# Kernel tuning notes

Measured on AMD Instinct MI355X. Metric: run time of the kernel, lower is better.

The kernel has to match this reference:

```python
import jax, jax.numpy as jnp
import numpy as np

B, H, W, D = 16, 48, 48, 384
EPS = 1e-5


def setup_inputs() -> dict:
    key = jax.random.key(0)
    ks = jax.random.split(key, 7)
    s_in = 1.0 / np.sqrt(D)
    s_pos = 1.0 / np.sqrt(2.0)
    return {
        "x": jax.random.normal(ks[0], (B, H, W, D), dtype=jnp.float32),
        "Wp": jax.random.uniform(ks[1], (2, D), minval=-s_pos, maxval=s_pos, dtype=jnp.float32),
        "bp": jax.random.uniform(ks[2], (D,), minval=-s_pos, maxval=s_pos, dtype=jnp.float32),
        "W1": jax.random.uniform(ks[3], (D, D), minval=-s_in, maxval=s_in, dtype=jnp.float32),
        "b1": jax.random.uniform(ks[4], (D,), minval=-s_in, maxval=s_in, dtype=jnp.float32),
        "W2": jax.random.uniform(ks[5], (D, D), minval=-s_in, maxval=s_in, dtype=jnp.float32),
        "b2": jax.random.uniform(ks[6], (D,), minval=-s_in, maxval=s_in, dtype=jnp.float32),
    }


def reference(x, Wp, bp, W1, b1, W2, b2):
    b, h, w, d = x.shape
    # positional encoding: (h, w, 2) -> Linear(2, d)
    ph = jnp.arange(h, dtype=jnp.float32)[:, None] * jnp.ones((1, w), jnp.float32)
    pw = jnp.arange(w, dtype=jnp.float32)[None, :] * jnp.ones((h, 1), jnp.float32)
    pos = jnp.stack((ph, pw), axis=-1)  # (h, w, 2)
    pos_enc = pos @ Wp + bp  # (h, w, d)
    x = x + pos_enc[None]
    xf = x.reshape(b, h * w, d)
    # unscaled self-attention: softmax(x x^T) x
    scores = jnp.einsum("bnd,bmd->bnm", xf, xf)  # (b, hw, hw)
    attn = jax.nn.softmax(scores, axis=-1)
    out = jnp.einsum("bnm,bmd->bnd", attn, xf)  # (b, hw, d)
    # MLP: Linear -> ReLU -> Linear
    out = jax.nn.relu(out @ W1 + b1) @ W2 + b2
    out = out.reshape(b, h, w, d) + x
    # layer_norm over [h, w, d] (no affine params)
    mean = jnp.mean(out, axis=(1, 2, 3), keepdims=True)
    var = jnp.var(out, axis=(1, 2, 3), keepdims=True)
    return (out - mean) * jax.lax.rsqrt(var + EPS)
```

## Files before the change

kernel.cpp:

```cpp
#include <hip/hip_runtime.h>
#include <cstdio>
#include <cstdint>

#define BB 16
#define HH 48
#define WW 48
#define DD 384
#define NTOK 2304
#define EPS 1e-5f
#define SZB 28311552u

typedef __attribute__((ext_vector_type(4))) float f32x4;
typedef __attribute__((ext_vector_type(8))) short bf16x8;
typedef __attribute__((ext_vector_type(4))) short bf16x4;

__device__ __forceinline__ unsigned short f2bf(float f) {
  uint32_t u = __float_as_uint(f);
  uint32_t r = (u + 0x7FFFu + ((u >> 16) & 1u)) >> 16;
  return (unsigned short)r;
}
__device__ __forceinline__ float bf2f(short s) {
  return __uint_as_float(((uint32_t)(unsigned short)s) << 16);
}

typedef __attribute__((address_space(3))) uint32_t lds_u32;
typedef __attribute__((address_space(1))) const uint32_t glob_u32;
__device__ __forceinline__ void gload_lds16(const void* g, void* l) {
  __builtin_amdgcn_global_load_lds((glob_u32*)g, (lds_u32*)l, 16, 0, 0);
}

__global__ void k_prep(const float* __restrict__ x, const float* __restrict__ Wp,
                       const float* __restrict__ bp, short* __restrict__ xhi,
                       short* __restrict__ xlo) {
  size_t e = ((size_t)blockIdx.x * 256 + threadIdx.x) * 4;
  int d = (int)(e % DD);
  int n = (int)((e / DD) % NTOK);
  float fh = (float)(n / WW), fw = (float)(n % WW);
  f32x4 v = *(const f32x4*)(x + e);
  bf16x4 hv, lv;
#pragma unroll
  for (int j = 0; j < 4; ++j) {
    float pe = fh * Wp[d + j] + fw * Wp[DD + d + j] + bp[d + j];
    float val = v[j] + pe;
    unsigned short hb = f2bf(val);
    hv[j] = (short)hb;
    lv[j] = (short)f2bf(val - bf2f((short)hb));
  }
  *(bf16x4*)(xhi + e) = hv;
  *(bf16x4*)(xlo + e) = lv;
}

__global__ void k_vfrag(const short* __restrict__ xhi, short* __restrict__ vfrag) {
  __shared__ __attribute__((aligned(16))) short tile[32 * 392];
  const int b = blockIdx.y, pt = blockIdx.x, tid = threadIdx.x;
  const short* src = xhi + ((size_t)b * NTOK + pt * 32) * DD;
#pragma unroll
  for (int c = 0; c < 6; ++c) {
    int u = c * 256 + tid;
    int r = u / 48, c8 = u % 48;
    *(bf16x8*)(&tile[r * 392 + c8 * 8]) = *(const bf16x8*)(src + (size_t)r * DD + c8 * 8);
  }
  __syncthreads();
  char* dst = (char*)vfrag + ((size_t)b * 72 + pt) * 24576;
#pragma unroll
  for (int c = 0; c < 6; ++c) {
    int u = c * 256 + tid;
    int db = u >> 6, l = u & 63, l15 = l & 15, lgv = l >> 4;
    bf16x8 vv;
#pragma unroll
    for (int j = 0; j < 8; ++j) {
      int tok = (j < 4) ? (lgv * 4 + j) : (16 + lgv * 4 + (j - 4));
      vv[j] = tile[tok * 392 + db * 16 + l15];
    }
    *(bf16x8*)(dst + (size_t)u * 16) = vv;
  }
}

__global__ void k_wprep(const float* __restrict__ W1, const float* __restrict__ W2,
                        short* __restrict__ w1t, short* __restrict__ w2t) {
  int idx = blockIdx.x * 256 + threadIdx.x;
  int r = idx / DD, c = idx % DD;
  w1t[c * DD + r] = (short)f2bf(W1[idx]);
  w2t[c * DD + r] = (short)f2bf(W2[idx]);
}

#define NTILE 144
#define NPAIR 72

__global__ __launch_bounds__(384, 2)
void k_attn(const short* __restrict__ xhi, const short* __restrict__ xlo,
            const short* __restrict__ vfrag, short* __restrict__ aout, int b0) {
  __shared__ __attribute__((aligned(16))) char lds_all[122880];
  const int tid = threadIdx.x;
  const int lane = tid & 63, wave = tid >> 6;
  const int ln15 = lane & 15, lg = lane >> 4;
  const int b = b0 + (blockIdx.x & 7);
  const int qt = blockIdx.x >> 3;
  const int q0 = qt * 96;
  const int swz = (ln15 & 7) << 4;

  uint32_t srcoff[4];
#pragma unroll
  for (int c = 0; c < 4; ++c) {
    int g = c * 6144 + tid * 16;
    int region = (g >= 12288) ? 1 : 0;
    int rem = g - region * 12288;
    int row = rem / 768;
    int col = rem - row * 768;
    srcoff[c] = (uint32_t)(row * 768 + (col ^ ((row & 7) << 4))) + (region ? SZB : 0u);
  }
  const char* kbp = (const char*)xhi + (size_t)b * NTOK * 768;
  const char* vbp = (const char*)vfrag + (size_t)b * 1769472;

  bf16x8 qh[12], ql[12];
  {
    const short* qp = xhi + ((size_t)b * NTOK + q0 + wave * 16 + ln15) * DD + lg * 8;
    const short* qlp = xlo + ((size_t)b * NTOK + q0 + wave * 16 + ln15) * DD + lg * 8;
#pragma unroll
    for (int kf = 0; kf < 12; ++kf) {
      qh[kf] = *(const bf16x8*)(qp + kf * 32);
      ql[kf] = *(const bf16x8*)(qlp + kf * 32);
    }
  }

  f32x4 o[24];
#pragma unroll
  for (int i = 0; i < 24; ++i) o[i] = f32x4{0.f, 0.f, 0.f, 0.f};
  float m1 = -INFINITY, l1 = 0.0f;

  char* bA = lds_all;
  char* bB = lds_all + 24576;
  char* bC = lds_all + 49152;
  char* vA = lds_all + 73728;
  char* vB = lds_all + 98304;

#pragma unroll
  for (int c = 0; c < 4; ++c) gload_lds16(kbp + srcoff[c], bA + c * 6144 + tid * 16);
#pragma unroll
  for (int c = 0; c < 4; ++c) gload_lds16(kbp + 12288 + srcoff[c], bB + c * 6144 + tid * 16);
#pragma unroll
  for (int c = 0; c < 4; ++c) gload_lds16(vbp + c * 6144 + tid * 16, vA + c * 6144 + tid * 16);
  asm volatile("s_waitcnt vmcnt(8)" ::: "memory");
  __builtin_amdgcn_s_barrier();
  __builtin_amdgcn_sched_barrier(0);

#pragma unroll 1
  for (int p = 0; p < NPAIR; ++p) {
    if (2 * p + 2 < NTILE) {
      const char* kn = kbp + (size_t)(2 * p + 2) * 12288;
#pragma unroll
      for (int c = 0; c < 4; ++c) gload_lds16(kn + srcoff[c], bC + c * 6144 + tid * 16);
    }
    f32x4 shh = f32x4{0.f, 0.f, 0.f, 0.f}, shl = shh, slh = shh;
    __builtin_amdgcn_s_setprio(1);
#pragma unroll
    for (int kf = 0; kf < 12; ++kf) {
      const int ca = (kf * 64 + lg * 16) ^ swz;
      bf16x8 ah = *(const bf16x8*)(bA + ln15 * 768 + ca);
      bf16x8 al = *(const bf16x8*)(bA + 12288 + ln15 * 768 + ca);
      shh = __builtin_amdgcn_mfma_f32_16x16x32_bf16(ah, qh[kf], shh, 0, 0, 0);
      shl = __builtin_amdgcn_mfma_f32_16x16x32_bf16(ah, ql[kf], shl, 0, 0, 0);
      slh = __builtin_amdgcn_mfma_f32_16x16x32_bf16(al, qh[kf], slh, 0, 0, 0);
    }
    __builtin_amdgcn_s_setprio(0);
    f32x4 sE;
#pragma unroll
    for (int r = 0; r < 4; ++r) sE[r] = shh[r] + shl[r] + slh[r];

    if (p + 1 < NPAIR) {
      asm volatile("s_waitcnt vmcnt(4)" ::: "memory");
    } else {
      asm volatile("s_waitcnt vmcnt(0)" ::: "memory");
    }
    __builtin_amdgcn_s_barrier();
    __builtin_amdgcn_sched_barrier(0);

    if (2 * p + 3 < NTILE) {
      const char* kn = kbp + (size_t)(2 * p + 3) * 12288;
#pragma unroll
      for (int c = 0; c < 4; ++c) gload_lds16(kn + srcoff[c], bA + c * 6144 + tid * 16);
    }
    if (p + 1 < NPAIR) {
      const char* vn = vbp + (size_t)(p + 1) * 24576;
#pragma unroll
      for (int c = 0; c < 4; ++c) gload_lds16(vn + c * 6144 + tid * 16, vB + c * 6144 + tid * 16);
    }
    shh = f32x4{0.f, 0.f, 0.f, 0.f}; shl = shh; slh = shh;
    __builtin_amdgcn_s_setprio(1);
#pragma unroll
    for (int kf = 0; kf < 12; ++kf) {
      const int ca = (kf * 64 + lg * 16) ^ swz;
      bf16x8 ah = *(const bf16x8*)(bB + ln15 * 768 + ca);
      bf16x8 al = *(const bf16x8*)(bB + 12288 + ln15 * 768 + ca);
      shh = __builtin_amdgcn_mfma_f32_16x16x32_bf16(ah, qh[kf], shh, 0, 0, 0);
      shl = __builtin_amdgcn_mfma_f32_16x16x32_bf16(ah, ql[kf], shl, 0, 0, 0);
      slh = __builtin_amdgcn_mfma_f32_16x16x32_bf16(al, qh[kf], slh, 0, 0, 0);
    }
    __builtin_amdgcn_s_setprio(0);
    f32x4 sO;
#pragma unroll
    for (int r = 0; r < 4; ++r) sO[r] = shh[r] + shl[r] + slh[r];

    float tmax = -INFINITY;
#pragma unroll
    for (int r = 0; r < 4; ++r) tmax = fmaxf(tmax, fmaxf(sE[r], sO[r]));
    tmax = fmaxf(tmax, __shfl_xor(tmax, 16));
    tmax = fmaxf(tmax, __shfl_xor(tmax, 32));
    if (__any(tmax - m1 > 8.f)) {
      float mn = fmaxf(m1, tmax);
      float al_ = __expf(m1 - mn);
      float alr[4];
#pragma unroll
      for (int r = 0; r < 4; ++r) alr[r] = __shfl(al_, lg * 4 + r);
#pragma unroll
      for (int ob = 0; ob < 24; ++ob)
#pragma unroll
        for (int r = 0; r < 4; ++r) o[ob][r] *= alr[r];
      l1 *= al_;
      m1 = mn;
    }
    float rs = 0.0f;
    bf16x8 p8;
#pragma unroll
    for (int r = 0; r < 4; ++r) {
      float pe = __expf(sE[r] - m1);
      float po = __expf(sO[r] - m1);
      rs += pe + po;
      p8[r] = (short)f2bf(pe);
      p8[r + 4] = (short)f2bf(po);
    }
    rs += __shfl_xor(rs, 16);
    rs += __shfl_xor(rs, 32);
    l1 += rs;

    const char* vt = vA + lane * 16;
    __builtin_amdgcn_s_setprio(1);
#pragma unroll
    for (int g = 0; g < 4; ++g) {
#pragma unroll
      for (int j = 0; j < 6; ++j) {
        bf16x8 vv = *(const bf16x8*)(vt + (g * 6 + j) * 1024);
        o[g * 6 + j] = __builtin_amdgcn_mfma_f32_16x16x32_bf16(p8, vv, o[g * 6 + j], 0, 0, 0);
      }
    }
    __builtin_amdgcn_s_setprio(0);

    asm volatile("s_waitcnt vmcnt(8)" ::: "memory");
    __builtin_amdgcn_s_barrier();
    __builtin_amdgcn_sched_barrier(0);

    char* t0 = bA;
    char* t1 = bB;
    bA = bC; bB = t0; bC = t1;
    char* tv = vA; vA = vB; vB = tv;
  }

  float lr[4];
#pragma unroll
  for (int r = 0; r < 4; ++r) lr[r] = __shfl(l1, lg * 4 + r);
  short* ob_ = aout + ((size_t)b * NTOK + q0 + wave * 16) * DD;
#pragma unroll
  for (int db = 0; db < 24; ++db) {
#pragma unroll
    for (int r = 0; r < 4; ++r) {
      float v = o[db][r] / lr[r];
      ob_[(size_t)(lg * 4 + r) * DD + db * 16 + ln15] = (short)f2bf(v);
    }
  }
}

__global__ __launch_bounds__(128, 3)
void k_mlp(const short* __restrict__ aout, const short* __restrict__ w1t,
           const short* __restrict__ w2t, const float* __restrict__ b1,
           const float* __restrict__ b2, const short* __restrict__ xhi,
           const short* __restrict__ xlo, short* __restrict__ ybf,
           float* __restrict__ stats) {
  __shared__ __attribute__((aligned(16))) short hid[2 * 16 * 392];
  __shared__ float redS[2], redQ[2];
  const int tid = threadIdx.x, lane = tid & 63, wave = tid >> 6;
  const int ln15 = lane & 15, lg = lane >> 4;
  const int row0 = blockIdx.x * 32;
  const int bb = row0 / NTOK;

  bf16x8 a[12];
  {
    const short* ap = aout + (size_t)(row0 + wave * 16 + ln15) * DD + lg * 8;
#pragma unroll
    for (int kf = 0; kf < 12; ++kf) a[kf] = *(const bf16x8*)(ap + kf * 32);
  }
  short* hw = &hid[wave * 16 * 392];
#pragma unroll 1
  for (int cb = 0; cb < 24; ++cb) {
    f32x4 acc = f32x4{0.f, 0.f, 0.f, 0.f};
#pragma unroll
    for (int kf = 0; kf < 12; ++kf) {
      bf16x8 wf = *(const bf16x8*)(w1t + (size_t)(cb * 16 + ln15) * DD + kf * 32 + lg * 8);
      acc = __builtin_amdgcn_mfma_f32_16x16x32_bf16(a[kf], wf, acc, 0, 0, 0);
    }
    float bias = b1[cb * 16 + ln15];
#pragma unroll
    for (int r = 0; r < 4; ++r) {
      float v = fmaxf(acc[r] + bias, 0.0f);
      hw[(lg * 4 + r) * 392 + cb * 16 + ln15] = (short)f2bf(v);
    }
  }
  __syncthreads();
  bf16x8 h[12];
#pragma unroll
  for (int kf = 0; kf < 12; ++kf)
    h[kf] = *(const bf16x8*)(&hw[ln15 * 392 + kf * 32 + lg * 8]);
  float ts = 0.f, tq = 0.f;
#pragma unroll 1
  for (int cb = 0; cb < 24; ++cb) {
    f32x4 acc = f32x4{0.f, 0.f, 0.f, 0.f};
#pragma unroll
    for (int kf = 0; kf < 12; ++kf) {
      bf16x8 wf = *(const bf16x8*)(w2t + (size_t)(cb * 16 + ln15) * DD + kf * 32 + lg * 8);
      acc = __builtin_amdgcn_mfma_f32_16x16x32_bf16(h[kf], wf, acc, 0, 0, 0);
    }
    int col = cb * 16 + ln15;
    float bias = b2[col];
#pragma unroll
    for (int r = 0; r < 4; ++r) {
      size_t row = (size_t)row0 + wave * 16 + lg * 4 + r;
      size_t idx = row * DD + col;
      float xv = bf2f(xhi[idx]) + bf2f(xlo[idx]);
      float y = acc[r] + bias + xv;
      ybf[idx] = (short)f2bf(y);
      ts += y;
      tq += y * y;
    }
  }
#pragma unroll
  for (int off = 32; off; off >>= 1) {
    ts += __shfl_xor(ts, off);
    tq += __shfl_xor(tq, off);
  }
  if (lane == 0) { redS[wave] = ts; redQ[wave] = tq; }
  __syncthreads();
  if (tid == 0) {
    atomicAdd(&stats[bb], redS[0] + redS[1]);
    atomicAdd(&stats[16 + bb], redQ[0] + redQ[1]);
  }
}

__global__ void k_ln(const short* __restrict__ ybf, float* __restrict__ out,
                     const float* __restrict__ stats) {
  size_t i8 = ((size_t)blockIdx.x * 256 + threadIdx.x) * 8;
  int b = (int)(i8 / ((size_t)NTOK * DD));
  const float cnt = (float)(NTOK * DD);
  float mean = stats[b] / cnt;
  float var = stats[16 + b] / cnt - mean * mean;
  float inv = rsqrtf(var + EPS);
  bf16x8 v = *(const bf16x8*)(ybf + i8);
  f32x4 o0, o1;
#pragma unroll
  for (int j = 0; j < 4; ++j) {
    o0[j] = (bf2f(v[j]) - mean) * inv;
    o1[j] = (bf2f(v[j + 4]) - mean) * inv;
  }
  *(f32x4*)(out + i8) = o0;
  *(f32x4*)(out + i8 + 4) = o1;
}

extern "C" void kernel_launch(void* const* d_in, const int* in_sizes, int n_in,
                              void* d_out, int out_size, void* d_ws, size_t ws_size,
                              hipStream_t stream) {
  const float* x  = (const float*)d_in[0];
  const float* Wp = (const float*)d_in[1];
  const float* bp = (const float*)d_in[2];
  const float* W1 = (const float*)d_in[3];
  const float* b1 = (const float*)d_in[4];
  const float* W2 = (const float*)d_in[5];
  const float* b2 = (const float*)d_in[6];
  float* out = (float*)d_out;

  const size_t SZ = (size_t)SZB;
  char* ws = (char*)d_ws;
  short* xhi   = (short*)ws;
  short* xlo   = (short*)(ws + SZ);
  short* vfrag = (short*)(ws + 2 * SZ);
  short* aout  = (short*)(ws + 3 * SZ);
  short* w1t   = (short*)(ws + 4 * SZ);
  short* w2t   = (short*)(ws + 4 * SZ + 294912);
  float* stats = (float*)(ws + 4 * SZ + 2 * 294912);
  const size_t need = 4 * SZ + 2 * 294912 + 128;
  if (ws_size < need) {
    fprintf(stderr, "kernel_launch: ws_size %zu < needed %zu\n", ws_size, need);
  }

  k_prep<<<13824, 256, 0, stream>>>(x, Wp, bp, xhi, xlo);
  k_vfrag<<<dim3(72, 16), 256, 0, stream>>>(xhi, vfrag);
  k_wprep<<<576, 256, 0, stream>>>(W1, W2, w1t, w2t);
  k_attn<<<192, 384, 0, stream>>>(xhi, xlo, vfrag, aout, 0);
  k_attn<<<192, 384, 0, stream>>>(xhi, xlo, vfrag, aout, 8);
  hipMemsetAsync(stats, 0, 32 * sizeof(float), stream);
  k_mlp<<<1152, 128, 0, stream>>>(aout, w1t, w2t, b1, b2, xhi, xlo, aout, stats);
  k_ln<<<6912, 256, 0, stream>>>(aout, out, stats);
}
```

Baseline: 668.2 us.

## Fuse prep into vfrag kernel and merge two attention launches into one

The positional-encoding add and hi/lo bf16 split now happen inside the V-fragment transpose kernel, so xhi no longer has to be written and then read back by a second pass. The two 192-block attention launches become one 384-block launch, with the block index remapped so blocks stay grouped by XCD and batch. This removes a launch and a full-tensor round trip, and removes the tail gap between the two attention launches. The fused prep reads fp32 scalars per element rather than as vectors, which may coalesce less well.

```diff
diff --git a/kernel.cpp b/kernel.cpp
--- a/kernel.cpp
+++ b/kernel.cpp
@@ -31,34 +31,33 @@
 
 __global__ void k_prep(const float* __restrict__ x, const float* __restrict__ Wp,
                        const float* __restrict__ bp, short* __restrict__ xhi,
-                       short* __restrict__ xlo) {
-  size_t e = ((size_t)blockIdx.x * 256 + threadIdx.x) * 4;
-  int d = (int)(e % DD);
-  int n = (int)((e / DD) % NTOK);
-  float fh = (float)(n / WW), fw = (float)(n % WW);
-  f32x4 v = *(const f32x4*)(x + e);
-  bf16x4 hv, lv;
-#pragma unroll
-  for (int j = 0; j < 4; ++j) {
-    float pe = fh * Wp[d + j] + fw * Wp[DD + d + j] + bp[d + j];
-    float val = v[j] + pe;
-    unsigned short hb = f2bf(val);
-    hv[j] = (short)hb;
-    lv[j] = (short)f2bf(val - bf2f((short)hb));
-  }
-  *(bf16x4*)(xhi + e) = hv;
-  *(bf16x4*)(xlo + e) = lv;
-}
-
-__global__ void k_vfrag(const short* __restrict__ xhi, short* __restrict__ vfrag) {
+                       short* __restrict__ xlo, short* __restrict__ vfrag) {
   __shared__ __attribute__((aligned(16))) short tile[32 * 392];
   const int b = blockIdx.y, pt = blockIdx.x, tid = threadIdx.x;
-  const short* src = xhi + ((size_t)b * NTOK + pt * 32) * DD;
+  const int n0 = pt * 32;
+  const float* src = x + ((size_t)b * NTOK + n0) * DD;
+  short* hdst = xhi + ((size_t)b * NTOK + n0) * DD;
+  short* ldst = xlo + ((size_t)b * NTOK + n0) * DD;
 #pragma unroll
   for (int c = 0; c < 6; ++c) {
     int u = c * 256 + tid;
     int r = u / 48, c8 = u % 48;
-    *(bf16x8*)(&tile[r * 392 + c8 * 8]) = *(const bf16x8*)(src + (size_t)r * DD + c8 * 8);
+    int d0 = c8 * 8;
+    int n = n0 + r;
+    float fh = (float)(n / WW), fw = (float)(n % WW);
+    bf16x8 hv, lv;
+#pragma unroll
+    for (int j = 0; j < 8; ++j) {
+      int d = d0 + j;
+      float pe = fh * Wp[d] + fw * Wp[DD + d] + bp[d];
+      float val = src[(size_t)r * DD + d] + pe;
+      unsigned short hb = f2bf(val);
+      hv[j] = (short)hb;
+      lv[j] = (short)f2bf(val - bf2f((short)hb));
+    }
+    *(bf16x8*)(&tile[r * 392 + d0]) = hv;
+    *(bf16x8*)(hdst + (size_t)r * DD + d0) = hv;
+    *(bf16x8*)(ldst + (size_t)r * DD + d0) = lv;
   }
   __syncthreads();
   char* dst = (char*)vfrag + ((size_t)b * 72 + pt) * 24576;
@@ -89,13 +88,16 @@
 
 __global__ __launch_bounds__(384, 2)
 void k_attn(const short* __restrict__ xhi, const short* __restrict__ xlo,
-            const short* __restrict__ vfrag, short* __restrict__ aout, int b0) {
+            const short* __restrict__ vfrag, short* __restrict__ aout) {
   __shared__ __attribute__((aligned(16))) char lds_all[122880];
   const int tid = threadIdx.x;
   const int lane = tid & 63, wave = tid >> 6;
   const int ln15 = lane & 15, lg = lane >> 4;
-  const int b = b0 + (blockIdx.x & 7);
-  const int qt = blockIdx.x >> 3;
+  const int bid = blockIdx.x;
+  const int xcd = bid & 7, slot = bid >> 3;
+  const int half = (slot >= 24) ? 1 : 0;
+  const int b = xcd + 8 * half;
+  const int qt = slot - 24 * half;
   const int q0 = qt * 96;
   const int swz = (ln15 & 7) << 4;
 
@@ -389,11 +391,9 @@
     fprintf(stderr, "kernel_launch: ws_size %zu < needed %zu\n", ws_size, need);
   }
 
-  k_prep<<<13824, 256, 0, stream>>>(x, Wp, bp, xhi, xlo);
-  k_vfrag<<<dim3(72, 16), 256, 0, stream>>>(xhi, vfrag);
+  k_prep<<<dim3(72, 16), 256, 0, stream>>>(x, Wp, bp, xhi, xlo, vfrag);
   k_wprep<<<576, 256, 0, stream>>>(W1, W2, w1t, w2t);
-  k_attn<<<192, 384, 0, stream>>>(xhi, xlo, vfrag, aout, 0);
-  k_attn<<<192, 384, 0, stream>>>(xhi, xlo, vfrag, aout, 8);
+  k_attn<<<384, 384, 0, stream>>>(xhi, xlo, vfrag, aout);
   hipMemsetAsync(stats, 0, 32 * sizeof(float), stream);
   k_mlp<<<1152, 128, 0, stream>>>(aout, w1t, w2t, b1, b2, xhi, xlo, aout, stats);
   k_ln<<<6912, 256, 0, stream>>>(aout, out, stats);
```

Result: no change. 665.2 us (-0.5%).
